# Kernel tuning notes

Hardware: AMD Instinct MI355X
Metric: run time of the kernel (lower is better)

Reference implementation:

```python
import jax, jax.numpy as jnp
import numpy as np


def setup_inputs() -> dict:
    key = jax.random.key(0)
    ks = jax.random.split(key, 8)
    B, C, H, W = 4, 256, 64, 64
    Ci = C // 8  # inter_channels = 32
    x = jax.random.normal(ks[0], (B, C, H, W), dtype=jnp.float32)
    # 1x1 conv weights stored as [out, in] matrices (kernel size 1)
    sq = 1.0 / np.sqrt(C)
    Wq = jax.random.uniform(ks[1], (Ci, C), jnp.float32, -sq, sq)
    bq = jax.random.uniform(ks[2], (Ci,), jnp.float32, -sq, sq)
    Wk = jax.random.uniform(ks[3], (Ci, C), jnp.float32, -sq, sq)
    bk = jax.random.uniform(ks[4], (Ci,), jnp.float32, -sq, sq)
    Wv = jax.random.uniform(ks[5], (C, C), jnp.float32, -sq, sq)
    bv = jax.random.uniform(ks[6], (C,), jnp.float32, -sq, sq)
    # torch initializes gamma to zeros; use a nonzero value so output depends on attention path
    gamma = jnp.array([0.5], dtype=jnp.float32)
    return {"x": x, "Wq": Wq, "bq": bq, "Wk": Wk, "bk": bk, "Wv": Wv, "bv": bv, "gamma": gamma}


def reference(x, Wq, bq, Wk, bk, Wv, bv, gamma):
    B, C, H, W = x.shape
    N = H * W
    xf = x.reshape(B, C, N)                        # [B, C, N]
    # 1x1 convs == channel-mixing matmuls
    q = jnp.einsum('oc,bcn->bon', Wq, xf) + bq[None, :, None]   # [B, Ci, N]
    k = jnp.einsum('oc,bcn->bon', Wk, xf) + bk[None, :, None]   # [B, Ci, N]
    v = jnp.einsum('oc,bcn->bon', Wv, xf) + bv[None, :, None]   # [B, C,  N]
    # energy[b, n, m] = sum_c q[b, c, n] * k[b, c, m]  (no scaling, per DANet)
    energy = jnp.einsum('bcn,bcm->bnm', q, k)      # [B, N, N]
    attention = jax.nn.softmax(energy, axis=-1)    # softmax over keys m
    # out[b, c, n] = sum_m v[b, c, m] * attention[b, n, m]
    out = jnp.einsum('bcm,bnm->bcn', v, attention)
    out = out.reshape(B, C, H, W)
    return gamma[0] * out + x
```

## Files before the change

### kernel.cpp

```cpp
#include <hip/hip_runtime.h>
#include <hip/hip_bf16.h>
#include <math.h>

typedef __bf16 bf16x8 __attribute__((ext_vector_type(8)));
typedef float  floatx4 __attribute__((ext_vector_type(4)));
typedef float  floatx16 __attribute__((ext_vector_type(16)));
typedef unsigned u32x2 __attribute__((ext_vector_type(2)));

#define MFMA(a, b, c)   __builtin_amdgcn_mfma_f32_16x16x32_bf16((a), (b), (c), 0, 0, 0)
#define MFMA32(a, b, c) __builtin_amdgcn_mfma_f32_32x32x16_bf16((a), (b), (c), 0, 0, 0)

__device__ __forceinline__ unsigned short f2bf(float f) {
  union { float f; unsigned u; } v; v.f = f;
  unsigned r = v.u + 0x7FFFu + ((v.u >> 16) & 1u);
  return (unsigned short)(r >> 16);
}
__device__ __forceinline__ float bf2f(unsigned short u) {
  union { unsigned u; float f; } v; v.u = ((unsigned)u) << 16;
  return v.f;
}
__device__ __forceinline__ unsigned pack2(float a, float b) {
  __bf16 x = (__bf16)a, y = (__bf16)b;
  unsigned short ux = __builtin_bit_cast(unsigned short, x);
  unsigned short uy = __builtin_bit_cast(unsigned short, y);
  return (unsigned)ux | ((unsigned)uy << 16);
}

__global__ __launch_bounds__(256) void k_wconv(const float* __restrict__ Wq,
                                               const float* __restrict__ Wk,
                                               const float* __restrict__ Wv,
                                               unsigned short* __restrict__ Wall) {
  int i = blockIdx.x * 256 + threadIdx.x;
  int o = i >> 8, c = i & 255;
  float v = (o < 32) ? Wq[o * 256 + c]
          : (o < 64) ? Wk[(o - 32) * 256 + c]
                     : Wv[(o - 64) * 256 + c];
  Wall[i] = f2bf(v);
}

__global__ __launch_bounds__(256) void k_xpose(const float* __restrict__ x,
                                               unsigned short* __restrict__ xT) {
  int bid = blockIdx.x;
  int b = bid >> 8, rem = bid & 255;
  int nb = rem >> 2, cb = rem & 3;
  int n0 = nb * 64, c0 = cb * 64;
  int tid = threadIdx.x;
  __shared__ alignas(16) unsigned short T[64][72];
#pragma unroll
  for (int i = 0; i < 4; ++i) {
    int idx = tid + 256 * i;
    int r = idx >> 4, g = idx & 15;
    float4 d = *(const float4*)(x + ((size_t)b * 256 + c0 + r) * 4096 + n0 + g * 4);
    T[g * 4 + 0][r] = f2bf(d.x);
    T[g * 4 + 1][r] = f2bf(d.y);
    T[g * 4 + 2][r] = f2bf(d.z);
    T[g * 4 + 3][r] = f2bf(d.w);
  }
  __syncthreads();
#pragma unroll
  for (int i = 0; i < 2; ++i) {
    int idx = tid + 256 * i;
    int j = idx >> 3, g = idx & 7;
    *(uint4*)(xT + ((size_t)b * 4096 + n0 + j) * 256 + c0 + g * 8) =
        *(const uint4*)&T[j][g * 8];
  }
}

__global__ __launch_bounds__(64, 4) void k_proj(const unsigned short* __restrict__ xT,
                                                const unsigned short* __restrict__ Wall,
                                                const float* __restrict__ bq,
                                                const float* __restrict__ bk,
                                                const float* __restrict__ bv,
                                                unsigned short* __restrict__ qbf,
                                                unsigned short* __restrict__ kbf,
                                                unsigned short* __restrict__ vbf) {
  int b = blockIdx.x >> 9;
  int m0 = ((blockIdx.x >> 1) & 255) * 16;
  int h = blockIdx.x & 1;
  int lane = threadIdx.x & 63;
  int l15 = lane & 15, quad = lane >> 4;

  floatx4 acc[10];
#pragma unroll
  for (int tt = 0; tt < 10; ++tt) acc[tt] = floatx4{0.f, 0.f, 0.f, 0.f};

  const unsigned short* arow = xT + ((size_t)b * 4096 + m0 + l15) * 256;
#pragma unroll
  for (int ks = 0; ks < 8; ++ks) {
    bf16x8 a = *(const bf16x8*)(arow + ks * 32 + quad * 8);
#pragma unroll
    for (int tt = 0; tt < 10; ++tt) {
      int gt = (tt < 2) ? (h * 2 + tt) : (4 + h * 8 + (tt - 2));
      bf16x8 w = *(const bf16x8*)(Wall + (size_t)(gt * 16 + l15) * 256 + ks * 32 + quad * 8);
      acc[tt] = MFMA(a, w, acc[tt]);
    }
  }
#pragma unroll
  for (int tt = 0; tt < 2; ++tt) {
    int o = (h * 2 + tt) * 16 + l15;
    float bias = (o < 32) ? bq[o] : bk[o - 32];
    unsigned short* dst = (o < 32) ? qbf : kbf;
    int oc = o & 31;
#pragma unroll
    for (int r = 0; r < 4; ++r) {
      int m = m0 + quad * 4 + r;
      dst[((size_t)b * 4096 + m) * 32 + oc] = f2bf(acc[tt][r] + bias);
    }
  }
  __shared__ alignas(16) unsigned short Os[128][24];
#pragma unroll
  for (int tt = 2; tt < 10; ++tt) {
    int lr = (tt - 2) * 16 + l15;
    int c = h * 128 + lr;
    float bias = bv[c];
#pragma unroll
    for (int r = 0; r < 4; ++r)
      Os[lr][quad * 4 + r] = f2bf(acc[tt][r] + bias);
  }
  __syncthreads();
  {
    int nb = m0 >> 5, off = m0 & 31;
#pragma unroll
    for (int i = 0; i < 4; ++i) {
      int idx = threadIdx.x + 64 * i;
      int r = idx >> 1, g = idx & 1;
      int c = h * 128 + r;
      *(uint4*)(vbf + (((size_t)b * 128 + nb) * 256 + c) * 32 + off + g * 8) =
          *(const uint4*)&Os[r][g * 8];
    }
  }
}

__device__ __forceinline__ void softmax_pack(floatx16 st, float& lp, bf16x8 (&pa)[2], int hi) {
  float p[16];
#pragma unroll
  for (int r = 0; r < 16; ++r) p[r] = __expf(st[r]);
  lp += (((p[0] + p[1]) + (p[2] + p[3])) + ((p[4] + p[5]) + (p[6] + p[7]))) +
        (((p[8] + p[9]) + (p[10] + p[11])) + ((p[12] + p[13]) + (p[14] + p[15])));
  unsigned d0[4], d1[4];
#pragma unroll
  for (int t = 0; t < 4; ++t) {
    d0[t] = pack2(p[4 * t + 0], p[4 * t + 1]);
    d1[t] = pack2(p[4 * t + 2], p[4 * t + 3]);
  }
#pragma unroll
  for (int ks = 0; ks < 2; ++ks) {
#if __has_builtin(__builtin_amdgcn_permlane32_swap)
    (void)hi;
    u32x2 r0 = __builtin_amdgcn_permlane32_swap(d0[2 * ks], d0[2 * ks + 1], false, false);
    u32x2 r1 = __builtin_amdgcn_permlane32_swap(d1[2 * ks], d1[2 * ks + 1], false, false);
    union { unsigned u[4]; bf16x8 v; } u;
    u.u[0] = r0[0]; u.u[1] = r1[0]; u.u[2] = r0[1]; u.u[3] = r1[1];
    pa[ks] = u.v;
#else
    unsigned s0 = hi ? d0[2 * ks] : d0[2 * ks + 1];
    unsigned s1 = hi ? d1[2 * ks] : d1[2 * ks + 1];
    unsigned o0 = (unsigned)__shfl_xor((int)s0, 32);
    unsigned o1 = (unsigned)__shfl_xor((int)s1, 32);
    union { unsigned u[4]; bf16x8 v; } u;
    u.u[0] = hi ? o0 : d0[2 * ks];
    u.u[1] = hi ? o1 : d1[2 * ks];
    u.u[2] = hi ? d0[2 * ks + 1] : o0;
    u.u[3] = hi ? d1[2 * ks + 1] : o1;
    pa[ks] = u.v;
#endif
  }
}

__global__ __launch_bounds__(64, 2) void k_attn(const unsigned short* __restrict__ qbf,
                                                const unsigned short* __restrict__ kbf,
                                                const unsigned short* __restrict__ vbf,
                                                unsigned short* __restrict__ Obf,
                                                float* __restrict__ lsum) {
  int wg = (blockIdx.x & 7) * 256 + (blockIdx.x >> 3);
  const int qb = wg & 63;
  const int g  = wg >> 6;
  const int cw = g & 1;
  const int s  = (g >> 1) & 3;
  const int b  = g >> 3;
  const int lane = threadIdx.x & 63;
  const int l31 = lane & 31;
  const int hi  = lane >> 5;
  const int q0  = qb * 64;

  const floatx16 z16 = {0.f, 0.f, 0.f, 0.f, 0.f, 0.f, 0.f, 0.f,
                        0.f, 0.f, 0.f, 0.f, 0.f, 0.f, 0.f, 0.f};

  bf16x8 qf[2][2];
  {
    const unsigned short* qbase = qbf + ((size_t)b * 4096 + q0 + l31) * 32 + hi * 8;
#pragma unroll
    for (int qs2 = 0; qs2 < 2; ++qs2)
#pragma unroll
      for (int kh = 0; kh < 2; ++kh)
        qf[qs2][kh] = *(const bf16x8*)(qbase + qs2 * 32 * 32 + kh * 16);
  }

  floatx16 acc[2][4];
#pragma unroll
  for (int i = 0; i < 2; ++i)
#pragma unroll
    for (int j = 0; j < 4; ++j) acc[i][j] = z16;

  float lp0 = 0.f, lp1 = 0.f;

  const unsigned short* krow = kbf + ((size_t)b * 4096 + s * 1024 + l31) * 32 + hi * 8;
  const unsigned short* vrow =
      vbf + (((size_t)b * 128 + s * 32) * 256 + cw * 128 + l31) * 32 + hi * 8;

  bf16x8 kf0 = *(const bf16x8*)krow;
  bf16x8 kf1 = *(const bf16x8*)(krow + 16);

  for (int it = 0; it < 32; ++it) {
    bf16x8 vb[4][2];
    const unsigned short* vit = vrow + (size_t)it * 8192;
#pragma unroll
    for (int ct = 0; ct < 4; ++ct) {
      vb[ct][0] = *(const bf16x8*)(vit + ct * 1024);
      vb[ct][1] = *(const bf16x8*)(vit + ct * 1024 + 16);
    }
    const unsigned short* kn = krow + (size_t)((it + 1) & 31) * 1024;
    bf16x8 kn0 = *(const bf16x8*)kn;
    bf16x8 kn1 = *(const bf16x8*)(kn + 16);

    floatx16 st0 = MFMA32(kf0, qf[0][0], z16);
    st0 = MFMA32(kf1, qf[0][1], st0);
    floatx16 st1 = MFMA32(kf0, qf[1][0], z16);
    st1 = MFMA32(kf1, qf[1][1], st1);
    kf0 = kn0; kf1 = kn1;

    bf16x8 pa[2][2];
    softmax_pack(st0, lp0, pa[0], hi);
    softmax_pack(st1, lp1, pa[1], hi);

    __builtin_amdgcn_s_setprio(1);
#pragma unroll
    for (int ct = 0; ct < 4; ++ct) {
      acc[0][ct] = MFMA32(pa[0][0], vb[ct][0], acc[0][ct]);
      acc[1][ct] = MFMA32(pa[1][0], vb[ct][0], acc[1][ct]);
      acc[0][ct] = MFMA32(pa[0][1], vb[ct][1], acc[0][ct]);
      acc[1][ct] = MFMA32(pa[1][1], vb[ct][1], acc[1][ct]);
    }
    __builtin_amdgcn_s_setprio(0);
  }

  lp0 += __shfl_xor(lp0, 32);
  lp1 += __shfl_xor(lp1, 32);
  if (cw == 0) {
    float lv = hi ? lp1 : lp0;
    lsum[((size_t)s * 4 + b) * 4096 + q0 + hi * 32 + l31] = lv;
  }
#pragma unroll
  for (int qs2 = 0; qs2 < 2; ++qs2)
#pragma unroll
    for (int ct = 0; ct < 4; ++ct) {
      unsigned short* orow = Obf +
          (((size_t)s * 4 + b) * 256 + cw * 128 + ct * 32 + l31) * 4096 +
          q0 + qs2 * 32 + hi * 4;
#pragma unroll
      for (int gi = 0; gi < 4; ++gi) {
        unsigned w0 = pack2(acc[qs2][ct][4 * gi + 0], acc[qs2][ct][4 * gi + 1]);
        unsigned w1 = pack2(acc[qs2][ct][4 * gi + 2], acc[qs2][ct][4 * gi + 3]);
        unsigned long long w = (unsigned long long)w0 | ((unsigned long long)w1 << 32);
        *(unsigned long long*)(orow + 8 * gi) = w;
      }
    }
}

__global__ __launch_bounds__(256) void k_merge(const unsigned short* __restrict__ Obf,
                                               const float* __restrict__ lsum,
                                               const float* __restrict__ x,
                                               const float* __restrict__ gma,
                                               float* __restrict__ out) {
  int t = blockIdx.x * 256 + threadIdx.x;
  int n4 = t & 1023;
  int c = (t >> 10) & 255;
  int b = t >> 18;
  int n = n4 << 2;
  size_t xa = (((size_t)b * 256 + c) << 12) + n;
  float4 xv = *(const float4*)(x + xa);
  float L0 = 0.f, L1 = 0.f, L2 = 0.f, L3 = 0.f;
  float o0 = 0.f, o1 = 0.f, o2 = 0.f, o3 = 0.f;
#pragma unroll
  for (int s = 0; s < 4; ++s) {
    float4 ls = *(const float4*)(lsum + (((size_t)s * 4 + b) << 12) + n);
    L0 += ls.x; L1 += ls.y; L2 += ls.z; L3 += ls.w;
    ushort4 ov = *(const ushort4*)(Obf + ((((size_t)s * 4 + b) * 256 + c) << 12) + n);
    o0 += bf2f(ov.x); o1 += bf2f(ov.y); o2 += bf2f(ov.z); o3 += bf2f(ov.w);
  }
  float g = gma[0];
  float4 r;
  r.x = xv.x + g * o0 / L0;
  r.y = xv.y + g * o1 / L1;
  r.z = xv.z + g * o2 / L2;
  r.w = xv.w + g * o3 / L3;
  *(float4*)(out + xa) = r;
}

extern "C" void kernel_launch(void* const* d_in, const int* in_sizes, int n_in,
                              void* d_out, int out_size, void* d_ws, size_t ws_size,
                              hipStream_t stream) {
  const float* x   = (const float*)d_in[0];
  const float* Wq  = (const float*)d_in[1];
  const float* bq  = (const float*)d_in[2];
  const float* Wk  = (const float*)d_in[3];
  const float* bk  = (const float*)d_in[4];
  const float* Wv  = (const float*)d_in[5];
  const float* bv  = (const float*)d_in[6];
  const float* gma = (const float*)d_in[7];
  float* out = (float*)d_out;

  unsigned short* qbf  = (unsigned short*)d_ws;
  unsigned short* kbf  = qbf + (size_t)4 * 4096 * 32;
  unsigned short* vbf  = kbf + (size_t)4 * 4096 * 32;
  unsigned short* Wall = vbf + (size_t)4 * 128 * 256 * 32;
  unsigned short* xT   = Wall + (size_t)320 * 256;
  unsigned short* Obf  = xT;
  float* lsum = (float*)(Obf + (size_t)4 * 4 * 256 * 4096);

  k_wconv<<<320, 256, 0, stream>>>(Wq, Wk, Wv, Wall);
  k_xpose<<<1024, 256, 0, stream>>>(x, xT);
  k_proj<<<2048, 64, 0, stream>>>(xT, Wall, bq, bk, bv, qbf, kbf, vbf);
  k_attn<<<2048, 64, 0, stream>>>(qbf, kbf, vbf, Obf, lsum);
  k_merge<<<4096, 256, 0, stream>>>(Obf, lsum, x, gma, out);
}
```

Before: 175.7 us.

## Store Q/K/V in MFMA fragment-major layout and use exp2 with log2e-scaled Q

Q, K and V are now written by the projection kernel in a fragment-major tiled layout, so each lane's 16-byte operand load in the attention kernel is contiguous across lanes. This replaces the previous strided row-major loads and is meant to cut global memory transactions in the attention loop. Q is pre-scaled by log2(e) so the softmax can use the hardware exp2 instruction instead of __expf, which saves a multiply per element. The scaled Q is rounded to bf16, which slightly changes the attention logits.

```diff
diff --git a/kernel.cpp b/kernel.cpp
--- a/kernel.cpp
+++ b/kernel.cpp
@@ -24,6 +24,13 @@
   unsigned short ux = __builtin_bit_cast(unsigned short, x);
   unsigned short uy = __builtin_bit_cast(unsigned short, y);
   return (unsigned)ux | ((unsigned)uy << 16);
+}
+__device__ __forceinline__ float exp2_fast(float x) {
+#if __has_builtin(__builtin_amdgcn_exp2f)
+  return __builtin_amdgcn_exp2f(x);
+#else
+  return exp2f(x);
+#endif
 }
 
 __global__ __launch_bounds__(256) void k_wconv(const float* __restrict__ Wq,
@@ -99,12 +106,15 @@
   for (int tt = 0; tt < 2; ++tt) {
     int o = (h * 2 + tt) * 16 + l15;
     float bias = (o < 32) ? bq[o] : bk[o - 32];
+    float scale = (o < 32) ? 1.44269504088896340736f : 1.0f;
     unsigned short* dst = (o < 32) ? qbf : kbf;
     int oc = o & 31;
+    int kh = oc >> 4, h2 = (oc >> 3) & 1, c8 = oc & 7;
 #pragma unroll
     for (int r = 0; r < 4; ++r) {
       int m = m0 + quad * 4 + r;
-      dst[((size_t)b * 4096 + m) * 32 + oc] = f2bf(acc[tt][r] + bias);
+      dst[(size_t)b * 131072 + (size_t)(m >> 5) * 1024 + kh * 512 + h2 * 256 +
+          (m & 31) * 8 + c8] = f2bf((acc[tt][r] + bias) * scale);
     }
   }
   __shared__ alignas(16) unsigned short Os[128][24];
@@ -119,14 +129,17 @@
   }
   __syncthreads();
   {
-    int nb = m0 >> 5, off = m0 & 31;
+    int kb = m0 >> 5, kk = (m0 >> 4) & 1;
 #pragma unroll
     for (int i = 0; i < 4; ++i) {
       int idx = threadIdx.x + 64 * i;
-      int r = idx >> 1, g = idx & 1;
-      int c = h * 128 + r;
-      *(uint4*)(vbf + (((size_t)b * 128 + nb) * 256 + c) * 32 + off + g * 8) =
-          *(const uint4*)&Os[r][g * 8];
+      int cbl = idx >> 6;
+      int rem = idx & 63;
+      int h2 = rem >> 5, ch = rem & 31;
+      int r = cbl * 32 + ch;
+      *(uint4*)(vbf + (size_t)b * 1048576 + (size_t)kb * 8192 +
+                (size_t)(h * 4 + cbl) * 1024 + kk * 512 + h2 * 256 + ch * 8) =
+          *(const uint4*)&Os[r][h2 * 8];
     }
   }
 }
@@ -134,7 +147,7 @@
 __device__ __forceinline__ void softmax_pack(floatx16 st, float& lp, bf16x8 (&pa)[2], int hi) {
   float p[16];
 #pragma unroll
-  for (int r = 0; r < 16; ++r) p[r] = __expf(st[r]);
+  for (int r = 0; r < 16; ++r) p[r] = exp2_fast(st[r]);
   lp += (((p[0] + p[1]) + (p[2] + p[3])) + ((p[4] + p[5]) + (p[6] + p[7]))) +
         (((p[8] + p[9]) + (p[10] + p[11])) + ((p[12] + p[13]) + (p[14] + p[15])));
   unsigned d0[4], d1[4];
@@ -188,12 +201,13 @@
 
   bf16x8 qf[2][2];
   {
-    const unsigned short* qbase = qbf + ((size_t)b * 4096 + q0 + l31) * 32 + hi * 8;
+    const unsigned short* qbase =
+        qbf + (size_t)b * 131072 + (size_t)(qb * 2) * 1024 + hi * 256 + l31 * 8;
 #pragma unroll
     for (int qs2 = 0; qs2 < 2; ++qs2)
 #pragma unroll
       for (int kh = 0; kh < 2; ++kh)
-        qf[qs2][kh] = *(const bf16x8*)(qbase + qs2 * 32 * 32 + kh * 16);
+        qf[qs2][kh] = *(const bf16x8*)(qbase + qs2 * 1024 + kh * 512);
   }
 
   floatx16 acc[2][4];
@@ -204,12 +218,14 @@
 
   float lp0 = 0.f, lp1 = 0.f;
 
-  const unsigned short* krow = kbf + ((size_t)b * 4096 + s * 1024 + l31) * 32 + hi * 8;
+  const unsigned short* krow =
+      kbf + (size_t)b * 131072 + (size_t)(s * 32) * 1024 + hi * 256 + l31 * 8;
   const unsigned short* vrow =
-      vbf + (((size_t)b * 128 + s * 32) * 256 + cw * 128 + l31) * 32 + hi * 8;
+      vbf + (size_t)b * 1048576 + (size_t)(s * 32) * 8192 + (size_t)(cw * 4) * 1024 +
+      hi * 256 + l31 * 8;
 
   bf16x8 kf0 = *(const bf16x8*)krow;
-  bf16x8 kf1 = *(const bf16x8*)(krow + 16);
+  bf16x8 kf1 = *(const bf16x8*)(krow + 512);
 
   for (int it = 0; it < 32; ++it) {
     bf16x8 vb[4][2];
@@ -217,11 +233,11 @@
 #pragma unroll
     for (int ct = 0; ct < 4; ++ct) {
       vb[ct][0] = *(const bf16x8*)(vit + ct * 1024);
-      vb[ct][1] = *(const bf16x8*)(vit + ct * 1024 + 16);
+      vb[ct][1] = *(const bf16x8*)(vit + ct * 1024 + 512);
     }
     const unsigned short* kn = krow + (size_t)((it + 1) & 31) * 1024;
     bf16x8 kn0 = *(const bf16x8*)kn;
-    bf16x8 kn1 = *(const bf16x8*)(kn + 16);
+    bf16x8 kn1 = *(const bf16x8*)(kn + 512);
 
     floatx16 st0 = MFMA32(kf0, qf[0][0], z16);
     st0 = MFMA32(kf1, qf[0][1], st0);
@@ -311,9 +327,9 @@
   float* out = (float*)d_out;
 
   unsigned short* qbf  = (unsigned short*)d_ws;
-  unsigned short* kbf  = qbf + (size_t)4 * 4096 * 32;
-  unsigned short* vbf  = kbf + (size_t)4 * 4096 * 32;
-  unsigned short* Wall = vbf + (size_t)4 * 128 * 256 * 32;
+  unsigned short* kbf  = qbf + (size_t)4 * 131072;
+  unsigned short* vbf  = kbf + (size_t)4 * 131072;
+  unsigned short* Wall = vbf + (size_t)4 * 1048576;
   unsigned short* xT   = Wall + (size_t)320 * 256;
   unsigned short* Obf  = xT;
   float* lsum = (float*)(Obf + (size_t)4 * 4 * 256 * 4096);
```

Result: faster. 170.5 us (-3.0%).
